# Kernel tuning notes

Hardware: AMD Instinct MI355X
Metric: run time of the kernel (lower is better)

## Reference

```python
import jax, jax.numpy as jnp
import numpy as np
import math

D_MODEL = 1024
NHEAD = 16
D_K = D_MODEL // NHEAD
LAMDA_ATT = 1.0
B, L = 2, 2048


def setup_inputs() -> dict:
    key = jax.random.key(0)
    ks = jax.random.split(key, 10)
    s = 1.0 / math.sqrt(D_MODEL)
    x = jax.random.normal(ks[0], (B, L, D_MODEL), dtype=jnp.float32)
    delta_r = jax.random.uniform(ks[1], (B, L), dtype=jnp.float32)  # positive, fed to log
    Wq = jax.random.normal(ks[2], (D_MODEL, D_MODEL), dtype=jnp.float32) * s
    Wk = jax.random.normal(ks[3], (D_MODEL, D_MODEL), dtype=jnp.float32) * s
    Wv = jax.random.normal(ks[4], (D_MODEL, D_MODEL), dtype=jnp.float32) * s
    Wo = jax.random.normal(ks[5], (D_MODEL, D_MODEL), dtype=jnp.float32) * s
    bq = jnp.zeros((D_MODEL,), jnp.float32)
    bk = jnp.zeros((D_MODEL,), jnp.float32)
    bv = jnp.zeros((D_MODEL,), jnp.float32)
    bo = jnp.zeros((D_MODEL,), jnp.float32)
    return {"x": x, "delta_r": delta_r, "Wq": Wq, "bq": bq, "Wk": Wk, "bk": bk,
            "Wv": Wv, "bv": bv, "Wo": Wo, "bo": bo}


def reference(x, delta_r, Wq, bq, Wk, bk, Wv, bv, Wo, bo):
    b, l, d = x.shape
    h, dk = NHEAD, D_K

    def proj(y, W, bias):
        # [B,L,D] -> [B,H,L,dk]
        return (y @ W + bias).reshape(b, l, h, dk).transpose(0, 2, 1, 3)

    v_scaled = x * delta_r[..., None]
    q = proj(x, Wq, bq)
    k = proj(x, Wk, bk)
    v = proj(v_scaled, Wv, bv)

    scores = jnp.einsum('bhqd,bhkd->bhqk', q, k) / math.sqrt(dk)
    pos = jnp.arange(l)
    dist = jnp.abs(pos[None, :] - pos[:, None]).astype(scores.dtype)  # [L,L]
    rel_bias = LAMDA_ATT * jnp.log(delta_r + 1e-6)  # [B,L]
    scores = scores - dist[None, None] * 0.1 + rel_bias[:, None, None, :]

    attn = jax.nn.softmax(scores, axis=-1)  # dropout is identity in eval mode
    context = jnp.einsum('bhqk,bhkd->bqhd', attn, v).reshape(b, l, d)
    out = context @ Wo + bo
    return out, attn.mean(axis=1)
```

## Files before the change

kernel.cpp:

```cpp
#include <hip/hip_runtime.h>
#include <math.h>

#define DMODEL 1024
#define NHEAD  16
#define DK     64
#define BB     2
#define LL     2048
#define MTOT   (BB*LL)

#define LOG2E      1.4426950408889634f
#define SCQ        (0.125f * LOG2E)
#define C2LOG      (0.1f * LOG2E)
#define SKIP_BOUND (-24.0f)

typedef __bf16 bf16_t;
typedef __bf16 bf16x8 __attribute__((ext_vector_type(8)));
typedef __bf16 bf16x4 __attribute__((ext_vector_type(4)));
typedef float  f32x4  __attribute__((ext_vector_type(4)));

static __device__ __forceinline__ f32x4 mfma16(bf16x8 a, bf16x8 b, f32x4 c) {
    return __builtin_amdgcn_mfma_f32_16x16x32_bf16(a, b, c, 0, 0, 0);
}
static __device__ __forceinline__ float exp2f_fast(float x) {
    return __builtin_amdgcn_exp2f(x);
}
static __device__ __forceinline__ float log2f_fast(float x) {
    return __builtin_amdgcn_logf(x);
}
static __device__ __forceinline__ void gl_lds16(const bf16_t* g, bf16_t* l) {
    __builtin_amdgcn_global_load_lds(
        (const __attribute__((address_space(1))) unsigned int*)g,
        (__attribute__((address_space(3))) unsigned int*)l, 16, 0, 0);
}

__global__ __launch_bounds__(256) void prep_fused_k(
    const float* __restrict__ x, const float* __restrict__ dr,
    bf16_t* __restrict__ xb, float* __restrict__ logd2,
    const float* __restrict__ Wq, const float* __restrict__ Wk,
    const float* __restrict__ Wv, const float* __restrict__ Wo,
    bf16_t* __restrict__ Wcat, bf16_t* __restrict__ Wot)
{
    __shared__ __align__(16) float Ts[64][68];
    const int bid = blockIdx.x;
    const int tid = threadIdx.x;
    if (bid < 2048) {
        size_t gid = (size_t)bid * 256 + tid;
        size_t off = gid * 8;
        float4 a = *(const float4*)(x + off);
        float4 c = *(const float4*)(x + off + 4);
        float va[8] = {a.x, a.y, a.z, a.w, c.x, c.y, c.z, c.w};
        bf16x8 o1;
#pragma unroll
        for (int j = 0; j < 8; ++j) o1[j] = (bf16_t)va[j];
        *(bf16x8*)(xb + off) = o1;
        if (gid < MTOT) logd2[gid] = log2f_fast(dr[gid] + 1e-6f);
    } else {
        const int t = bid - 2048;
        const int z = t >> 8;
        const float* W = (z == 0) ? Wq : (z == 1) ? Wk : (z == 2) ? Wv : Wo;
        bf16_t* dst = (z < 3) ? (Wcat + (size_t)z * DMODEL * DMODEL) : Wot;
        const int k0 = (t & 15) * 64, n0 = ((t >> 4) & 15) * 64;
#pragma unroll
        for (int i = 0; i < 4; ++i) {
            int u = tid + 256 * i, r = u >> 4, c4 = (u & 15) * 4;
            *(float4*)&Ts[r][c4] = *(const float4*)(W + (size_t)(k0 + r) * DMODEL + n0 + c4);
        }
        __syncthreads();
#pragma unroll
        for (int i = 0; i < 2; ++i) {
            int u = tid + 256 * i, n = u >> 3, k8 = (u & 7) * 8;
            bf16x8 v;
#pragma unroll
            for (int j = 0; j < 8; ++j) v[j] = (bf16_t)Ts[k8 + j][n];
            *(bf16x8*)(dst + (size_t)(n0 + n) * DMODEL + k0 + k8) = v;
        }
    }
}

__global__ __launch_bounds__(256, 3) void gemm128_k(
    const bf16_t* __restrict__ A, const bf16_t* __restrict__ Bt,
    const float* __restrict__ b0, const float* __restrict__ b1,
    const float* __restrict__ b2, const float* __restrict__ delta,
    bf16_t* __restrict__ outQ, bf16_t* __restrict__ outK,
    bf16_t* __restrict__ outVt, bf16_t* __restrict__ outQf,
    bf16_t* __restrict__ outKf)
{
    __shared__ __align__(16) bf16_t Asw[128 * 64];
    __shared__ __align__(16) bf16_t Bsw[128 * 64];
    const int tid = threadIdx.x, lane = tid & 63, w = tid >> 6;
    const int quad = lane >> 4, n16 = lane & 15;
    const int wm = (w & 1) * 64, wn = (w >> 1) * 64;
    const int m0 = blockIdx.y * 128, n0 = blockIdx.x * 128;
    const int srow = lane >> 3;
    const int scb  = (lane & 7) ^ srow;

    f32x4 acc[4][4] = {};

    for (int K0 = 0; K0 < DMODEL; K0 += 64) {
        __syncthreads();
#pragma unroll
        for (int i = 0; i < 4; ++i) {
            int rb = w * 32 + i * 8;
            gl_lds16(A  + (size_t)(m0 + rb + srow) * DMODEL + K0 + scb * 8,
                     &Asw[rb * 64]);
            gl_lds16(Bt + (size_t)(n0 + rb + srow) * DMODEL + K0 + scb * 8,
                     &Bsw[rb * 64]);
        }
        __syncthreads();
#pragma unroll
        for (int kc = 0; kc < 2; ++kc) {
            const int pcb = ((kc * 4 + quad) ^ (n16 & 7)) * 8;
            bf16x8 af[4], bfv[4];
#pragma unroll
            for (int mi = 0; mi < 4; ++mi)
                af[mi] = *(const bf16x8*)&Asw[(wm + mi * 16 + n16) * 64 + pcb];
#pragma unroll
            for (int ni = 0; ni < 4; ++ni)
                bfv[ni] = *(const bf16x8*)&Bsw[(wn + ni * 16 + n16) * 64 + pcb];
#pragma unroll
            for (int mi = 0; mi < 4; ++mi)
#pragma unroll
                for (int ni = 0; ni < 4; ++ni)
                    acc[mi][ni] = mfma16(af[mi], bfv[ni], acc[mi][ni]);
        }
    }

    const int region = n0 >> 10;
    if (region == 2) {
#pragma unroll
        for (int mi = 0; mi < 4; ++mi) {
            const int mbase = m0 + wm + mi * 16 + quad * 4;
            const int bidx = mbase >> 11, l = mbase & (LL - 1);
            const f32x4 dm4 = *(const f32x4*)(delta + mbase);
#pragma unroll
            for (int ni = 0; ni < 4; ++ni) {
                const int nl = (n0 & 1023) + wn + ni * 16 + n16;
                const int h = nl >> 6, dd = nl & 63;
                const float bv = b2[nl];
                bf16x4 pk;
#pragma unroll
                for (int r = 0; r < 4; ++r)
                    pk[r] = (bf16_t)(acc[mi][ni][r] * dm4[r] + bv);
                *(bf16x4*)(outVt + ((size_t)(bidx * NHEAD + h) * DK + dd) * LL + l) = pk;
            }
        }
    } else {
        const float* bias = (region == 0) ? b0 : b1;
        bf16_t* dst = (region == 0) ? outQ : outK;
        bf16_t* fdst = (region == 0) ? outQf : outKf;
        const float qs = (region == 0) ? SCQ : 1.0f;
#pragma unroll
        for (int mi = 0; mi < 4; ++mi) {
#pragma unroll
            for (int r = 0; r < 4; ++r) {
                const int m = m0 + wm + mi * 16 + quad * 4 + r;
                const int bidx = m >> 11, l = m & (LL - 1);
#pragma unroll
                for (int ni = 0; ni < 4; ++ni) {
                    const int nl = (n0 & 1023) + wn + ni * 16 + n16;
                    const int h = nl >> 6, dd = nl & 63;
                    float v = (acc[mi][ni][r] + bias[nl]) * qs;
                    bf16_t bv16 = (bf16_t)v;
                    dst[(((size_t)(bidx * NHEAD + h) * LL) + l) * DK + dd] = bv16;
                    fdst[(((size_t)(bidx * NHEAD + h) * (LL >> 4) + (l >> 4)) * 8 +
                          (dd >> 5) * 4 + ((dd >> 3) & 3)) * 128 +
                         (l & 15) * 8 + (dd & 7)] = bv16;
                }
            }
        }
    }
}

__global__ __launch_bounds__(256) void stats_k(
    const bf16_t* __restrict__ Q, const bf16_t* __restrict__ K,
    const float* __restrict__ logd2, float* __restrict__ Qn,
    float* __restrict__ Kn, float* __restrict__ dlb, float* __restrict__ ldx)
{
    __shared__ float qn_s[256], kn_s[256], dg_s[256];
    const int blk = blockIdx.x;
    const int bh = blk >> 3, seg = blk & 7, b = bh >> 4;
    const int tid = threadIdx.x;
    const int row = seg * 256 + tid;
    const size_t base = (size_t)bh * LL * DK;

    float qn2 = 0.f, kn2 = 0.f, dg = 0.f;
#pragma unroll
    for (int j = 0; j < 8; ++j) {
        bf16x8 qv = *(const bf16x8*)(Q + base + (size_t)row * DK + j * 8);
        bf16x8 kv = *(const bf16x8*)(K + base + (size_t)row * DK + j * 8);
#pragma unroll
        for (int e = 0; e < 8; ++e) {
            float fq = (float)qv[e], fk = (float)kv[e];
            qn2 += fq * fq; kn2 += fk * fk; dg += fq * fk;
        }
    }
    qn_s[tid] = qn2;
    kn_s[tid] = kn2;
    dg_s[tid] = dg + logd2[b * LL + row];
    __syncthreads();

    if (tid < 2) {
        float mq = 0.f, md = 1e30f;
        for (int r = 0; r < 128; ++r) {
            mq = fmaxf(mq, qn_s[tid * 128 + r]);
            md = fminf(md, dg_s[tid * 128 + r]);
        }
        Qn[bh * 16 + seg * 2 + tid] = sqrtf(mq);
        dlb[bh * 16 + seg * 2 + tid] = md;
    } else if (tid >= 64 && tid < 68) {
        const int t = tid - 64;
        float mk = 0.f;
        for (int r = 0; r < 64; ++r) mk = fmaxf(mk, kn_s[t * 64 + r]);
        Kn[bh * 32 + seg * 4 + t] = sqrtf(mk);
    } else if (tid >= 128 && tid < 132 && (bh & 15) == 0) {
        const int t = tid - 128;
        float ml = -1e30f;
        for (int r = 0; r < 64; ++r)
            ml = fmaxf(ml, logd2[b * LL + seg * 256 + t * 64 + r]);
        ldx[b * 32 + seg * 4 + t] = ml;
    }
}

__global__ __launch_bounds__(256) void mlstat_k(
    const float* __restrict__ mlws, float* __restrict__ mlmin)
{
    __shared__ float s[2048];
    const int tid = threadIdx.x, bh = blockIdx.x;
#pragma unroll
    for (int i = 0; i < 8; ++i)
        s[tid + 256 * i] = mlws[(size_t)bh * LL + tid + 256 * i];
    __syncthreads();
    if (tid < 16) {
        float m = 1e30f;
        for (int r = 0; r < 128; ++r) m = fminf(m, s[tid * 128 + r]);
        mlmin[bh * 16 + tid] = m;
    }
}

__global__ __launch_bounds__(256, 4) void attn_flash_mfma_k(
    const bf16_t* __restrict__ Q, const bf16_t* __restrict__ K,
    const bf16_t* __restrict__ Vt, const float* __restrict__ logd2,
    const float* __restrict__ Qn, const float* __restrict__ Kn,
    const float* __restrict__ dlb, const float* __restrict__ ldx,
    bf16_t* __restrict__ ctx, float* __restrict__ mlout)
{
    __shared__ __align__(16) bf16_t Ks[64][72];
    __shared__ __align__(16) bf16_t Vts[64][72];
    __shared__ __align__(16) bf16_t Ps[4][16][72];
    __shared__ float logds[64];

    const int tid = threadIdx.x;
    const int lane = tid & 63, w = tid >> 6;
    const int quad = lane >> 4, n16 = lane & 15;
    const int bh = blockIdx.x, b = bh >> 4, h = bh & 15;
    const int qt = blockIdx.y, q0 = qt * 64;
    const size_t base = (size_t)bh * LL * DK;
    const int q = q0 + w * 16 + n16;

    bf16x8 qa[2];
#pragma unroll
    for (int kc = 0; kc < 2; ++kc)
        qa[kc] = *(const bf16x8*)(Q + base + (size_t)q * DK + kc * 32 + quad * 8);

    unsigned mask = 0;
    {
        const float qn = Qn[bh * 16 + (qt >> 1)], dl = dlb[bh * 16 + (qt >> 1)];
        for (int t = 0; t < 32; ++t) {
            const int kc0 = t * 64;
            const int dmin = (kc0 > q0 + 63) ? (kc0 - (q0 + 63))
                           : ((q0 > kc0 + 63) ? (q0 - (kc0 + 63)) : 0);
            const float bound = qn * Kn[bh * 32 + t] + ldx[b * 32 + t]
                              - C2LOG * (float)dmin - dl;
            if (bound > SKIP_BOUND) mask |= (1u << t);
        }
    }

    const int strow = tid >> 3, stc8 = (tid & 7) * 8;
    bf16x8 kr0, kr1, vr0, vr1;
    float ldr = 0.f;
    auto prefetch = [&](int k0) {
        kr0 = *(const bf16x8*)(K + base + (size_t)(k0 + strow) * DK + stc8);
        kr1 = *(const bf16x8*)(K + base + (size_t)(k0 + 32 + strow) * DK + stc8);
        vr0 = *(const bf16x8*)(Vt + base + (size_t)strow * LL + k0 + stc8);
        vr1 = *(const bf16x8*)(Vt + base + (size_t)(32 + strow) * LL + k0 + stc8);
        if (tid < 64) ldr = logd2[b * LL + k0 + tid];
    };

    float m_c = -1e30f, l_c = 0.f;
    f32x4 o[4] = {};
    const float dfq = (float)(q - quad * 4);

    int t = (int)__builtin_ctz(mask);
    prefetch(t * 64);
    for (;;) {
        const unsigned rem = (t < 31) ? (mask >> (t + 1)) : 0u;
        const int tn = rem ? (t + 1 + (int)__builtin_ctz(rem)) : -1;
        __syncthreads();
        *(bf16x8*)&Ks[strow][stc8]       = kr0;
        *(bf16x8*)&Ks[32 + strow][stc8]  = kr1;
        *(bf16x8*)&Vts[strow][stc8]      = vr0;
        *(bf16x8*)&Vts[32 + strow][stc8] = vr1;
        if (tid < 64) logds[tid] = ldr;
        __syncthreads();
        if (tn >= 0) prefetch(tn * 64);
        const int k0 = t * 64;

        f32x4 s[4] = {};
#pragma unroll
        for (int kc = 0; kc < 2; ++kc) {
#pragma unroll
            for (int kt = 0; kt < 4; ++kt) {
                bf16x8 kb = *(const bf16x8*)&Ks[kt * 16 + n16][kc * 32 + quad * 8];
                s[kt] = mfma16(kb, qa[kc], s[kt]);
            }
        }
        const float df = dfq - (float)k0;
#pragma unroll
        for (int kt = 0; kt < 4; ++kt) {
            f32x4 ldv = *(const f32x4*)&logds[kt * 16 + quad * 4];
#pragma unroll
            for (int r = 0; r < 4; ++r)
                s[kt][r] += ldv[r] - C2LOG * fabsf(df - (float)(kt * 16 + r));
        }
        f32x4 mx;
#pragma unroll
        for (int r = 0; r < 4; ++r)
            mx[r] = fmaxf(fmaxf(s[0][r], s[1][r]), fmaxf(s[2][r], s[3][r]));
        float rm = fmaxf(fmaxf(mx[0], mx[1]), fmaxf(mx[2], mx[3]));
        rm = fmaxf(rm, __shfl_xor(rm, 16));
        rm = fmaxf(rm, __shfl_xor(rm, 32));
        const float mn = fmaxf(m_c, rm);
        const float alpha = exp2f_fast(m_c - mn);
        if (__any(mn > m_c)) {
#pragma unroll
            for (int dt = 0; dt < 4; ++dt)
#pragma unroll
                for (int r = 0; r < 4; ++r) o[dt][r] *= alpha;
        }
        f32x4 ps = {0.f, 0.f, 0.f, 0.f};
#pragma unroll
        for (int kt = 0; kt < 4; ++kt)
#pragma unroll
            for (int r = 0; r < 4; ++r) {
                float p = exp2f_fast(s[kt][r] - mn);
                s[kt][r] = p;
                ps[r] += p;
            }
        float psum = (ps[0] + ps[1]) + (ps[2] + ps[3]);
        psum += __shfl_xor(psum, 16);
        psum += __shfl_xor(psum, 32);
        l_c = l_c * alpha + psum;
        m_c = mn;
#pragma unroll
        for (int kt = 0; kt < 4; ++kt) {
            bf16x4 pk;
#pragma unroll
            for (int r = 0; r < 4; ++r) pk[r] = (bf16_t)s[kt][r];
            *(bf16x4*)&Ps[w][n16][kt * 16 + quad * 4] = pk;
        }
        __threadfence_block();
#pragma unroll
        for (int kc = 0; kc < 2; ++kc) {
            bf16x8 pa = *(const bf16x8*)&Ps[w][n16][kc * 32 + quad * 8];
#pragma unroll
            for (int dt = 0; dt < 4; ++dt) {
                bf16x8 vb = *(const bf16x8*)&Vts[dt * 16 + n16][kc * 32 + quad * 8];
                o[dt] = mfma16(vb, pa, o[dt]);
            }
        }
        if (tn < 0) break;
        t = tn;
    }
    const float inv = 1.f / l_c;
#pragma unroll
    for (int dt = 0; dt < 4; ++dt) {
        bf16x4 ov;
#pragma unroll
        for (int r = 0; r < 4; ++r) ov[r] = (bf16_t)(o[dt][r] * inv);
        *(bf16x4*)(ctx + ((size_t)b * LL + q) * DMODEL + h * DK +
                   dt * 16 + quad * 4) = ov;
    }
    if (quad == 0)
        mlout[(size_t)bh * LL + q] = m_c + log2f_fast(l_c);
}

__global__ __launch_bounds__(256, 3) void tail_fused_k(
    const bf16_t* __restrict__ A, const bf16_t* __restrict__ Bt,
    const float* __restrict__ b0, float* __restrict__ outf,
    const bf16_t* __restrict__ Qf, const bf16_t* __restrict__ Kf,
    const float* __restrict__ logd2, const float* __restrict__ mlws,
    const float* __restrict__ Qn, const float* __restrict__ Kn,
    const float* __restrict__ mlmin, const float* __restrict__ ldx,
    float* __restrict__ outmean)
{
    __shared__ __align__(16) char smem[24576];

    const int bid = blockIdx.x;
    const int tid = threadIdx.x;
    const int lane = tid & 63, w = tid >> 6;
    const int quad = lane >> 4, n16 = lane & 15;

    if (bid >= 1024) {
        bf16_t* Asw = (bf16_t*)smem;
        bf16_t* Bsw = (bf16_t*)(smem + 8192);
        const int gb = bid - 1024;
        const int wm = (w & 1) * 32, wn = (w >> 1) * 64;
        const int m0 = (gb >> 3) * 64, n0 = (gb & 7) * 128;
        const int srow = lane >> 3;
        const int scb  = (lane & 7) ^ srow;

        f32x4 acc[2][4] = {};

        for (int K0 = 0; K0 < DMODEL; K0 += 64) {
            __syncthreads();
#pragma unroll
            for (int i = 0; i < 2; ++i) {
                int rb = w * 16 + i * 8;
                gl_lds16(A + (size_t)(m0 + rb + srow) * DMODEL + K0 + scb * 8,
                         &Asw[rb * 64]);
            }
#pragma unroll
            for (int i = 0; i < 4; ++i) {
                int rb = w * 32 + i * 8;
                gl_lds16(Bt + (size_t)(n0 + rb + srow) * DMODEL + K0 + scb * 8,
                         &Bsw[rb * 64]);
            }
            __syncthreads();
#pragma unroll
            for (int kc = 0; kc < 2; ++kc) {
                const int pcb = ((kc * 4 + quad) ^ (n16 & 7)) * 8;
                bf16x8 af[2], bfv[4];
#pragma unroll
                for (int mi = 0; mi < 2; ++mi)
                    af[mi] = *(const bf16x8*)&Asw[(wm + mi * 16 + n16) * 64 + pcb];
#pragma unroll
                for (int ni = 0; ni < 4; ++ni)
                    bfv[ni] = *(const bf16x8*)&Bsw[(wn + ni * 16 + n16) * 64 + pcb];
#pragma unroll
                for (int mi = 0; mi < 2; ++mi)
#pragma unroll
                    for (int ni = 0; ni < 4; ++ni)
                        acc[mi][ni] = mfma16(af[mi], bfv[ni], acc[mi][ni]);
            }
        }
#pragma unroll
        for (int mi = 0; mi < 2; ++mi) {
#pragma unroll
            for (int r = 0; r < 4; ++r) {
                const int m = m0 + wm + mi * 16 + quad * 4 + r;
#pragma unroll
                for (int ni = 0; ni < 4; ++ni) {
                    const int n = n0 + wn + ni * 16 + n16;
                    outf[(size_t)m * DMODEL + n] = acc[mi][ni][r] + b0[n];
                }
            }
        }
        return;
    }

    const int q0 = ((bid >> 5) & 15) * 128, b = bid >> 9;

    int ktile = 0;
    {
        const int c = q0 >> 6;
        int want = bid & 31;
        for (int d = 0; d < 32; ++d) {
            int ka = c - d, kb2 = c + 1 + d;
            if (ka >= 0 && ka < 32) {
                if (want == 0) { ktile = ka; break; }
                --want;
            }
            if (kb2 >= 0 && kb2 < 32) {
                if (want == 0) { ktile = kb2; break; }
                --want;
            }
        }
    }
    const int k0 = ktile * 64;
    const int qq[2] = {q0 + w * 32 + n16, q0 + w * 32 + 16 + n16};

    float bias0[2][4][4];
#pragma unroll
    for (int qg = 0; qg < 2; ++qg) {
        const float df = (float)(qq[qg] - k0 - quad * 4);
#pragma unroll
        for (int kt = 0; kt < 4; ++kt) {
            const f32x4 ldv = *(const f32x4*)(logd2 + b * LL + k0 + kt * 16 + quad * 4);
#pragma unroll
            for (int r = 0; r < 4; ++r)
                bias0[qg][kt][r] = ldv[r] - C2LOG * fabsf(df - (float)(kt * 16 + r));
        }
    }

    const int qt = q0 >> 7;
    const int dmin = (k0 > q0 + 127) ? (k0 - (q0 + 127))
                   : ((q0 > k0 + 63) ? (q0 - (k0 + 63)) : 0);
    unsigned hmask = 0;
    {
        const float dterm = ldx[b * 32 + ktile] - C2LOG * (float)dmin;
        for (int h = 0; h < NHEAD; ++h) {
            const int bh = b * 16 + h;
            const float bound = Qn[bh * 16 + qt] * Kn[bh * 32 + ktile] + dterm
                              - mlmin[bh * 16 + qt];
            if (bound > SKIP_BOUND) hmask |= (1u << h);
        }
    }

    f32x4 acc[2][4] = {};

    if (hmask) {
        const int kt16 = k0 >> 4;
        const int qt16 = (q0 >> 4) + w * 2;
        int h = (int)__builtin_ctz(hmask);
        for (;;) {
            const unsigned rem = (h < 15) ? (hmask >> (h + 1)) : 0u;
            const int hn = rem ? (h + 1 + (int)__builtin_ctz(rem)) : -1;
            const size_t hb = (size_t)(b * NHEAD + h) * LL * DK;

            const float ml0 = mlws[(size_t)(b * NHEAD + h) * LL + qq[0]];
            const float ml1 = mlws[(size_t)(b * NHEAD + h) * LL + qq[1]];

            f32x4 s[2][4] = {};
#pragma unroll
            for (int kc = 0; kc < 2; ++kc) {
                bf16x8 kbf[4];
#pragma unroll
                for (int kt = 0; kt < 4; ++kt)
                    kbf[kt] = *(const bf16x8*)(Kf + hb +
                              ((size_t)(kt16 + kt) * 8 + kc * 4 + quad) * 128 +
                              n16 * 8);
                const bf16x8 qc0 = *(const bf16x8*)(Qf + hb +
                              ((size_t)qt16 * 8 + kc * 4 + quad) * 128 + n16 * 8);
                const bf16x8 qc1 = *(const bf16x8*)(Qf + hb +
                              ((size_t)(qt16 + 1) * 8 + kc * 4 + quad) * 128 + n16 * 8);
#pragma unroll
                for (int kt = 0; kt < 4; ++kt) {
                    s[0][kt] = mfma16(kbf[kt], qc0, s[0][kt]);
                    s[1][kt] = mfma16(kbf[kt], qc1, s[1][kt]);
                }
            }
#pragma unroll
            for (int kt = 0; kt < 4; ++kt) {
#pragma unroll
                for (int r = 0; r < 4; ++r) {
                    acc[0][kt][r] += exp2f_fast(s[0][kt][r] + bias0[0][kt][r] - ml0);
                    acc[1][kt][r] += exp2f_fast(s[1][kt][r] + bias0[1][kt][r] - ml1);
                }
            }
            if (hn < 0) break;
            h = hn;
        }
    }

    const float invH = 1.f / (float)NHEAD;
#pragma unroll
    for (int qg = 0; qg < 2; ++qg)
#pragma unroll
        for (int kt = 0; kt < 4; ++kt) {
            f32x4 ov;
#pragma unroll
            for (int r = 0; r < 4; ++r) ov[r] = acc[qg][kt][r] * invH;
            *(f32x4*)(outmean + ((size_t)b * LL + qq[qg]) * LL + k0 +
                      kt * 16 + quad * 4) = ov;
        }
}

extern "C" void kernel_launch(void* const* d_in, const int* in_sizes, int n_in,
                              void* d_out, int out_size, void* d_ws, size_t ws_size,
                              hipStream_t stream) {
    const float* x  = (const float*)d_in[0];
    const float* dr = (const float*)d_in[1];
    const float* Wq = (const float*)d_in[2];
    const float* bq = (const float*)d_in[3];
    const float* Wk = (const float*)d_in[4];
    const float* bk = (const float*)d_in[5];
    const float* Wv = (const float*)d_in[6];
    const float* bv = (const float*)d_in[7];
    const float* Wo = (const float*)d_in[8];
    const float* bo = (const float*)d_in[9];
    float* out = (float*)d_out;
    char* ws = (char*)d_ws;
    const size_t MB = 1ull << 20;

    bf16_t* xb   = (bf16_t*)(ws);
    bf16_t* Wcat = (bf16_t*)(ws + 8 * MB);
    bf16_t* Wot  = (bf16_t*)(ws + 14 * MB);
    bf16_t* Qb   = (bf16_t*)(ws + 16 * MB);
    bf16_t* Kb   = (bf16_t*)(ws + 24 * MB);
    bf16_t* Vtb  = (bf16_t*)(ws + 32 * MB);
    float*  logd = (float*)(ws + 40 * MB);
    float*  mlws = (float*)(ws + 41 * MB);
    float*  Qns  = (float*)(ws + 42 * MB);
    float*  Kns  = (float*)(ws + 42 * MB + 4096);
    float*  dlb  = (float*)(ws + 42 * MB + 12288);
    float*  ldxp = (float*)(ws + 42 * MB + 16384);
    float*  mlmn = (float*)(ws + 42 * MB + 20480);
    bf16_t* Kf   = (bf16_t*)(ws + 43 * MB);
    bf16_t* Qf   = (bf16_t*)(ws + 51 * MB);
    bf16_t* ctx  = xb;

    prep_fused_k<<<3072, 256, 0, stream>>>(x, dr, xb, logd,
                                           Wq, Wk, Wv, Wo, Wcat, Wot);

    gemm128_k<<<dim3(24, 32), 256, 0, stream>>>(xb, Wcat, bq, bk, bv, dr,
                                                Qb, Kb, Vtb, Qf, Kf);
    stats_k<<<256, 256, 0, stream>>>(Qb, Kb, logd, Qns, Kns, dlb, ldxp);

    attn_flash_mfma_k<<<dim3(32, 32), 256, 0, stream>>>(Qb, Kb, Vtb, logd,
                                                        Qns, Kns, dlb, ldxp,
                                                        ctx, mlws);
    mlstat_k<<<32, 256, 0, stream>>>(mlws, mlmn);
    tail_fused_k<<<1536, 256, 0, stream>>>(ctx, Wot, bo, out,
                                           Qf, Kf, logd, mlws, Qns, Kns,
                                           mlmn, ldxp,
                                           out + (size_t)MTOT * DMODEL);
}
```

Baseline: 230.5 us.

## Split attention-mean tail into 32-row tiles with heads spread across waves

Result: no change. 230.0 us (-0.2%).

```diff
diff --git a/kernel.cpp b/kernel.cpp
--- a/kernel.cpp
+++ b/kernel.cpp
@@ -393,17 +393,17 @@
     const float* __restrict__ mlmin, const float* __restrict__ ldx,
     float* __restrict__ outmean)
 {
-    __shared__ __align__(16) char smem[24576];
+    __shared__ __align__(16) char smem[34816];
 
     const int bid = blockIdx.x;
     const int tid = threadIdx.x;
     const int lane = tid & 63, w = tid >> 6;
     const int quad = lane >> 4, n16 = lane & 15;
 
-    if (bid >= 1024) {
+    if (bid >= 4096) {
         bf16_t* Asw = (bf16_t*)smem;
         bf16_t* Bsw = (bf16_t*)(smem + 8192);
-        const int gb = bid - 1024;
+        const int gb = bid - 4096;
         const int wm = (w & 1) * 32, wn = (w >> 1) * 64;
         const int m0 = (gb >> 3) * 64, n0 = (gb & 7) * 128;
         const int srow = lane >> 3;
@@ -458,12 +458,14 @@
         return;
     }
 
-    const int q0 = ((bid >> 5) & 15) * 128, b = bid >> 9;
+    const int m = bid;
+    const int rank = m >> 7, bq = m & 127, b = bq >> 6, q32 = bq & 63;
+    const int q0 = q32 * 32;
 
     int ktile = 0;
     {
         const int c = q0 >> 6;
-        int want = bid & 31;
+        int want = rank;
         for (int d = 0; d < 32; ++d) {
             int ka = c - d, kb2 = c + 1 + d;
             if (ka >= 0 && ka < 32) {
@@ -477,23 +479,9 @@
         }
     }
     const int k0 = ktile * 64;
-    const int qq[2] = {q0 + w * 32 + n16, q0 + w * 32 + 16 + n16};
-
-    float bias0[2][4][4];
-#pragma unroll
-    for (int qg = 0; qg < 2; ++qg) {
-        const float df = (float)(qq[qg] - k0 - quad * 4);
-#pragma unroll
-        for (int kt = 0; kt < 4; ++kt) {
-            const f32x4 ldv = *(const f32x4*)(logd2 + b * LL + k0 + kt * 16 + quad * 4);
-#pragma unroll
-            for (int r = 0; r < 4; ++r)
-                bias0[qg][kt][r] = ldv[r] - C2LOG * fabsf(df - (float)(kt * 16 + r));
-        }
-    }
 
     const int qt = q0 >> 7;
-    const int dmin = (k0 > q0 + 127) ? (k0 - (q0 + 127))
+    const int dmin = (k0 > q0 + 31) ? (k0 - (q0 + 31))
                    : ((q0 > k0 + 63) ? (q0 - (k0 + 63)) : 0);
     unsigned hmask = 0;
     {
@@ -506,19 +494,41 @@
         }
     }
 
+    if (!hmask) {
+        const int row = tid >> 3, c8 = (tid & 7) * 8;
+        const f32x4 z = {0.f, 0.f, 0.f, 0.f};
+        float* dst = outmean + ((size_t)b * LL + q0 + row) * LL + k0 + c8;
+        *(f32x4*)dst = z;
+        *(f32x4*)(dst + 4) = z;
+        return;
+    }
+
+    const int qq0 = q0 + n16, qq1 = q0 + 16 + n16;
+
+    float bias0[2][4][4];
+#pragma unroll
+    for (int qg = 0; qg < 2; ++qg) {
+        const float df = (float)((qg ? qq1 : qq0) - k0 - quad * 4);
+#pragma unroll
+        for (int kt = 0; kt < 4; ++kt) {
+            const f32x4 ldv = *(const f32x4*)(logd2 + b * LL + k0 + kt * 16 + quad * 4);
+#pragma unroll
+            for (int r = 0; r < 4; ++r)
+                bias0[qg][kt][r] = ldv[r] - C2LOG * fabsf(df - (float)(kt * 16 + r));
+        }
+    }
+
     f32x4 acc[2][4] = {};
-
-    if (hmask) {
-        const int kt16 = k0 >> 4;
-        const int qt16 = (q0 >> 4) + w * 2;
-        int h = (int)__builtin_ctz(hmask);
-        for (;;) {
-            const unsigned rem = (h < 15) ? (hmask >> (h + 1)) : 0u;
-            const int hn = rem ? (h + 1 + (int)__builtin_ctz(rem)) : -1;
+    {
+        const int kt16 = k0 >> 4, qt16 = q0 >> 4;
+#pragma unroll
+        for (int i = 0; i < 4; ++i) {
+            const int h = w + i * 4;
+            if (!(hmask & (1u << h))) continue;
             const size_t hb = (size_t)(b * NHEAD + h) * LL * DK;
 
-            const float ml0 = mlws[(size_t)(b * NHEAD + h) * LL + qq[0]];
-            const float ml1 = mlws[(size_t)(b * NHEAD + h) * LL + qq[1]];
+            const float ml0 = mlws[(size_t)(b * NHEAD + h) * LL + qq0];
+            const float ml1 = mlws[(size_t)(b * NHEAD + h) * LL + qq1];
 
             f32x4 s[2][4] = {};
 #pragma unroll
@@ -547,22 +557,30 @@
                     acc[1][kt][r] += exp2f_fast(s[1][kt][r] + bias0[1][kt][r] - ml1);
                 }
             }
-            if (hn < 0) break;
-            h = hn;
-        }
-    }
+        }
+    }
+
+    float (*cmb)[32][68] = (float(*)[32][68])smem;
+#pragma unroll
+    for (int qg = 0; qg < 2; ++qg)
+#pragma unroll
+        for (int kt = 0; kt < 4; ++kt)
+            *(f32x4*)&cmb[w][qg * 16 + n16][kt * 16 + quad * 4] = acc[qg][kt];
+    __syncthreads();
 
     const float invH = 1.f / (float)NHEAD;
-#pragma unroll
-    for (int qg = 0; qg < 2; ++qg)
-#pragma unroll
-        for (int kt = 0; kt < 4; ++kt) {
-            f32x4 ov;
-#pragma unroll
-            for (int r = 0; r < 4; ++r) ov[r] = acc[qg][kt][r] * invH;
-            *(f32x4*)(outmean + ((size_t)b * LL + qq[qg]) * LL + k0 +
-                      kt * 16 + quad * 4) = ov;
-        }
+    const int row = tid >> 3, c8 = (tid & 7) * 8;
+    f32x4 s0 = {0.f, 0.f, 0.f, 0.f}, s1 = {0.f, 0.f, 0.f, 0.f};
+#pragma unroll
+    for (int w4 = 0; w4 < 4; ++w4) {
+        s0 += *(const f32x4*)&cmb[w4][row][c8];
+        s1 += *(const f32x4*)&cmb[w4][row][c8 + 4];
+    }
+#pragma unroll
+    for (int r = 0; r < 4; ++r) { s0[r] *= invH; s1[r] *= invH; }
+    float* dst = outmean + ((size_t)b * LL + q0 + row) * LL + k0 + c8;
+    *(f32x4*)dst = s0;
+    *(f32x4*)(dst + 4) = s1;
 }
 
 extern "C" void kernel_launch(void* const* d_in, const int* in_sizes, int n_in,
@@ -610,7 +628,7 @@
                                                         Qns, Kns, dlb, ldxp,
                                                         ctx, mlws);
     mlstat_k<<<32, 256, 0, stream>>>(mlws, mlmn);
-    tail_fused_k<<<1536, 256, 0, stream>>>(ctx, Wot, bo, out,
+    tail_fused_k<<<4608, 256, 0, stream>>>(ctx, Wot, bo, out,
                                            Qf, Kf, logd, mlws, Qns, Kns,
                                            mlmn, ldxp,
                                            out + (size_t)MTOT * DMODEL);
```
